# Kernel tuning notes

Measured on AMD Instinct MI355X. Metric: run time of the kernel, lower is better.

The kernel has to match this reference:

```python
import jax, jax.numpy as jnp
import numpy as np

B, C, H, W = 16, 256, 128, 512
MINW, MINH, AF, HS = 128, 32, 256, 256


def _conv1d(x, w, b, pad):
    # x (B, Cin, L), w (Cout, Cin, K) -> (B, Cout, L)
    y = jax.lax.conv_general_dilated(x, w, (1,), [(pad, pad)],
                                     dimension_numbers=('NCH', 'OIH', 'NCH'))
    return y + b[None, :, None]


def setup_inputs() -> dict:
    key = jax.random.key(0)
    ks = jax.random.split(key, 22)
    def p(i, shape, s=0.05):
        return jax.random.normal(ks[i], shape, jnp.float32) * s
    return dict(
        features=jax.random.normal(ks[0], (B, C, H, W), jnp.float32),
        prev_attn_weights=jax.random.uniform(ks[1], (B, H), jnp.float32),
        coverage_vector=jax.random.uniform(ks[2], (B, H), jnp.float32) * 2.0,
        hidden=jax.random.normal(ks[3], (2, 1, B, HS), jnp.float32),
        dw_w=p(4, (MINW, 1)), dw_b=p(5, (1,)),
        enc_w=p(6, (C, AF)), enc_b=p(7, (AF,)),
        conv_w=p(8, (16, 2, 15)), conv_b=p(9, (16,)),
        dcb_w=p(10, (16, AF)), dcb_b=p(11, (AF,)),
        hid_w=p(12, (HS, AF)), hid_b=p(13, (AF,)),
        align_w=p(14, (AF, 1)), align_b=p(15, (1,)),
        convd_w=p(16, (AF, AF, 5)), convd_b=p(17, (AF,)),
        dh_w=p(18, (MINH, 1)), dh_b=p(19, (1,)),
        dec_w=p(20, (HS + AF, 2)), dec_b=p(21, (2,)),
    )


def reference(features, prev_attn_weights, coverage_vector, hidden,
              dw_w, dw_b, enc_w, enc_b, conv_w, conv_b, dcb_w, dcb_b,
              hid_w, hid_b, align_w, align_b, convd_w, convd_b,
              dh_w, dh_b, dec_w, dec_b):
    b, c, h, w = features.shape
    # AdaptiveMaxPool2d((None, MINW)): W divisible by MINW -> uniform windows
    pooled = features.reshape(b, c, h, MINW, w // MINW).max(-1)   # (B,C,H,MINW)
    h_feat = (pooled @ dw_w + dw_b)[..., 0]                       # (B,C,H)
    s = jnp.einsum('bch,cf->bhf', h_feat, enc_w) + enc_b          # (B,H,AF)
    # location + clamped coverage, InstanceNorm1d (no affine, eps=1e-5)
    cat = jnp.stack([prev_attn_weights,
                     jnp.clip(coverage_vector, 0.0, 1.0)], axis=1)  # (B,2,H)
    mu = cat.mean(-1, keepdims=True)
    var = cat.var(-1, keepdims=True)
    cat = (cat - mu) * jax.lax.rsqrt(var + 1e-5)
    cb = _conv1d(cat, conv_w, conv_b, 7)                          # (B,16,H)
    s = s + jnp.einsum('bkh,kf->bhf', cb, dcb_w) + dcb_b
    hh = hidden[0]                                                # (1,B,HS) = LSTM h
    s = s + (jnp.einsum('lbh,hf->lbf', hh, hid_w) + hid_b).transpose(1, 0, 2)  # (B,1,AF) bcast
    s = jnp.tanh(s)
    align = s @ align_w + align_b                                 # (B,H,1)
    attn = jax.nn.softmax(align, axis=1)[..., 0]                  # (B,H)
    context = jnp.einsum('bchw,bh->bcw', features, attn)          # (B,C,W)
    # learned stop decision
    d = jax.nn.relu(_conv1d(s.transpose(0, 2, 1), convd_w, convd_b, 2))  # (B,AF,H)
    d = d.reshape(b, AF, MINH, h // MINH).max(-1)                 # AdaptiveMaxPool1d(MINH)
    d = jax.nn.relu(d @ dh_w + dh_b)[..., 0]                      # (B,AF)
    d = jnp.concatenate([hh[0], d], axis=1)                       # (B,HS+AF)
    decision = d @ dec_w + dec_b                                  # (B,2)
    return context, attn, decision
```

## Files before the change

### kernel.cpp

```cpp
#include <hip/hip_runtime.h>
#include <hip/hip_bf16.h>
#include <math.h>

#define B_ 16
#define C_ 256
#define H_ 128
#define W_ 512
#define AF_ 256
#define HS_ 256

__global__ void k_pre(const float* __restrict__ convd_w,
                      const float* __restrict__ hidden,
                      const float* __restrict__ hid_w,
                      const float* __restrict__ hid_b,
                      float* __restrict__ w2, float* __restrict__ hv) {
  int bid = blockIdx.x, tid = threadIdx.x;
  if (bid < 256) {
    int f = bid;
#pragma unroll
    for (int q = 0; q < 5; ++q) {
      int r = q * 256 + tid;
      w2[(size_t)r * 256 + f] = convd_w[(size_t)f * 1280 + r];
    }
  } else {
    int b = bid - 256;
    const float* hh = hidden + b * HS_;
    float acc = hid_b[tid];
    for (int k = 0; k < HS_; ++k) acc = fmaf(hh[k], hid_w[k * AF_ + tid], acc);
    hv[b * AF_ + tid] = acc;
  }
}

__global__ void k_pool(const float* __restrict__ feat,
                       const float* __restrict__ dw_w,
                       const float* __restrict__ dw_b,
                       float* __restrict__ hf) {
  int gid = blockIdx.x * blockDim.x + threadIdx.x;
  int wid = gid >> 6;
  int lane = threadIdx.x & 63;
  const float4* row = reinterpret_cast<const float4*>(feat) + (size_t)wid * 128;
  float4 a = row[lane];
  float4 b = row[lane + 64];
  float m0 = fmaxf(fmaxf(a.x, a.y), fmaxf(a.z, a.w));
  float m1 = fmaxf(fmaxf(b.x, b.y), fmaxf(b.z, b.w));
  float p = m0 * dw_w[lane] + m1 * dw_w[lane + 64];
#pragma unroll
  for (int off = 32; off > 0; off >>= 1) p += __shfl_down(p, off, 64);
  if (lane == 0) hf[wid] = p + dw_b[0];
}

__global__ void k_sbuild(const float* __restrict__ pa,
                         const float* __restrict__ cv,
                         const float* __restrict__ hf,
                         const float* __restrict__ enc_w, const float* __restrict__ enc_b,
                         const float* __restrict__ conv_w, const float* __restrict__ conv_b,
                         const float* __restrict__ dcb_w, const float* __restrict__ dcb_b,
                         const float* __restrict__ hv,
                         const float* __restrict__ align_w, const float* __restrict__ align_b,
                         float* __restrict__ sbuf, float* __restrict__ alignv) {
  __shared__ float cat[2][H_];
  __shared__ float stats[4];
  __shared__ float cbl[4][16];
  __shared__ float red[4][4];
  int bidx = blockIdx.x;
  int b = bidx >> 5;
  int h0 = (bidx & 31) * 4;
  int tid = threadIdx.x;

  if (tid < H_) {
    cat[0][tid] = pa[b * H_ + tid];
    float x = cv[b * H_ + tid];
    cat[1][tid] = fminf(fmaxf(x, 0.f), 1.f);
  }
  __syncthreads();
  if (tid < 2) {
    float s = 0.f, s2 = 0.f;
    for (int t = 0; t < H_; ++t) { float x = cat[tid][t]; s += x; s2 += x * x; }
    float mu = s / (float)H_;
    float var = s2 / (float)H_ - mu * mu;
    stats[tid * 2] = mu;
    stats[tid * 2 + 1] = rsqrtf(var + 1e-5f);
  }
  __syncthreads();
  {
    int ch = tid >> 7, t = tid & 127;
    cat[ch][t] = (cat[ch][t] - stats[ch * 2]) * stats[ch * 2 + 1];
  }
  __syncthreads();
  if (tid < 64) {
    int k = tid & 15, j = tid >> 4;
    int h = h0 + j;
    float acc = conv_b[k];
    for (int c2 = 0; c2 < 2; ++c2)
      for (int t = 0; t < 15; ++t) {
        int hh = h + t - 7;
        if (hh >= 0 && hh < H_) acc += cat[c2][hh] * conv_w[(k * 2 + c2) * 15 + t];
      }
    cbl[j][k] = acc;
  }
  __syncthreads();

  int f = tid;
  float base = enc_b[f] + dcb_b[f] + hv[b * AF_ + f];
  float acc[4];
#pragma unroll
  for (int j = 0; j < 4; ++j) {
    float a = base;
#pragma unroll
    for (int k = 0; k < 16; ++k) a = fmaf(cbl[j][k], dcb_w[k * AF_ + f], a);
    acc[j] = a;
  }
  const float* hfb = hf + (size_t)(b * C_) * H_ + h0;
  for (int c = 0; c < C_; ++c) {
    float w = enc_w[c * AF_ + f];
#pragma unroll
    for (int j = 0; j < 4; ++j) acc[j] = fmaf(hfb[c * H_ + j], w, acc[j]);
  }
  float aw = align_w[f];
  int wvi = tid >> 6, lane = tid & 63;
#pragma unroll
  for (int j = 0; j < 4; ++j) {
    float s = tanhf(acc[j]);
    sbuf[(size_t)(b * H_ + h0 + j) * AF_ + f] = s;
    float v = s * aw;
#pragma unroll
    for (int off = 32; off > 0; off >>= 1) v += __shfl_down(v, off, 64);
    if (lane == 0) red[wvi][j] = v;
  }
  __syncthreads();
  if (tid < 4)
    alignv[b * H_ + h0 + tid] =
        red[0][tid] + red[1][tid] + red[2][tid] + red[3][tid] + align_b[0];
}

__global__ void k_softmax(const float* __restrict__ alignv, float* __restrict__ attn) {
  __shared__ float redm[2], reds[2];
  int b = blockIdx.x, t = threadIdx.x;
  float v = alignv[b * H_ + t];
  float m = v;
#pragma unroll
  for (int off = 32; off > 0; off >>= 1) m = fmaxf(m, __shfl_down(m, off, 64));
  if ((t & 63) == 0) redm[t >> 6] = m;
  __syncthreads();
  float mm = fmaxf(redm[0], redm[1]);
  float e = expf(v - mm);
  float s = e;
#pragma unroll
  for (int off = 32; off > 0; off >>= 1) s += __shfl_down(s, off, 64);
  if ((t & 63) == 0) reds[t >> 6] = s;
  __syncthreads();
  attn[b * H_ + t] = e / (reds[0] + reds[1]);
}

__global__ void k_dconv(const float* __restrict__ sbuf, const float* __restrict__ w2,
                        const float* __restrict__ convd_b, float* __restrict__ dpool) {
  __shared__ float sw[12][AF_];
  __shared__ float part[8][AF_];
  int bidx = blockIdx.x;
  int b = bidx >> 4;
  int h0 = (bidx & 15) * 8;
  int tid = threadIdx.x;
  int f = tid & 255;
  int chalf = tid >> 8;
  for (int rr = chalf; rr < 12; rr += 2) {
    int h = h0 - 2 + rr;
    sw[rr][f] = (h >= 0 && h < H_) ? sbuf[(size_t)(b * H_ + h) * AF_ + f] : 0.f;
  }
  __syncthreads();
  float acc[8];
#pragma unroll
  for (int j = 0; j < 8; ++j) acc[j] = 0.f;
  int cstart = chalf * 128;
  for (int c = cstart; c < cstart + 128; ++c) {
    float sr[12];
#pragma unroll
    for (int rr = 0; rr < 12; ++rr) sr[rr] = sw[rr][c];
    const float* wp = w2 + (size_t)c * 5 * 256 + f;
#pragma unroll
    for (int t = 0; t < 5; ++t) {
      float wv = wp[t * 256];
#pragma unroll
      for (int j = 0; j < 8; ++j) acc[j] = fmaf(sr[j + t], wv, acc[j]);
    }
  }
  if (chalf == 1) {
#pragma unroll
    for (int j = 0; j < 8; ++j) part[j][f] = acc[j];
  }
  __syncthreads();
  if (chalf == 0) {
    float bias = convd_b[f];
#pragma unroll
    for (int j = 0; j < 8; ++j) acc[j] = fmaxf(acc[j] + part[j][f] + bias, 0.f);
    float p0 = fmaxf(fmaxf(acc[0], acc[1]), fmaxf(acc[2], acc[3]));
    float p1 = fmaxf(fmaxf(acc[4], acc[5]), fmaxf(acc[6], acc[7]));
    int m0 = h0 >> 2;
    dpool[(size_t)(b * 32 + m0) * AF_ + f] = p0;
    dpool[(size_t)(b * 32 + m0 + 1) * AF_ + f] = p1;
  }
}

__global__ void k_decision(const float* __restrict__ dpool, const float* __restrict__ hidden,
                           const float* __restrict__ dh_w, const float* __restrict__ dh_b,
                           const float* __restrict__ dec_w, const float* __restrict__ dec_b,
                           float* __restrict__ dec_out) {
  __shared__ float ddl[AF_];
  __shared__ float red[4];
  int b = blockIdx.x, tid = threadIdx.x;
  float acc = dh_b[0];
  for (int m = 0; m < 32; ++m) acc = fmaf(dpool[(size_t)(b * 32 + m) * AF_ + tid], dh_w[m], acc);
  ddl[tid] = fmaxf(acc, 0.f);
  __syncthreads();
  int col = tid >> 7, kk = tid & 127;
  float a = 0.f;
#pragma unroll
  for (int q = 0; q < 4; ++q) {
    int idx = kk + 128 * q;
    float x = (idx < 256) ? hidden[b * HS_ + idx] : ddl[idx - 256];
    a = fmaf(x, dec_w[idx * 2 + col], a);
  }
#pragma unroll
  for (int off = 32; off > 0; off >>= 1) a += __shfl_down(a, off, 64);
  if ((tid & 63) == 0) red[tid >> 6] = a;
  __syncthreads();
  if (tid < 2) dec_out[b * 2 + tid] = red[tid * 2] + red[tid * 2 + 1] + dec_b[tid];
}

__global__ void k_context(const float* __restrict__ feat, const float* __restrict__ attn,
                          float* __restrict__ ctx) {
  __shared__ float at[H_];
  int cb = 2047 - blockIdx.x;
  int b = cb >> 7;
  int c0 = (cb & 127) * 2;
  int tid = threadIdx.x;
  if (tid < H_) at[tid] = attn[b * H_ + tid];
  __syncthreads();
  int c = c0 + (tid >> 7);
  int wq = tid & 127;
  const float4* f4 = reinterpret_cast<const float4*>(feat) +
                     (size_t)(b * C_ + c) * H_ * (W_ / 4) + wq;
  float4 acc = make_float4(0.f, 0.f, 0.f, 0.f);
  for (int h = 0; h < H_; ++h) {
    float4 x = f4[(size_t)h * (W_ / 4)];
    float a = at[h];
    acc.x += x.x * a; acc.y += x.y * a; acc.z += x.z * a; acc.w += x.w * a;
  }
  reinterpret_cast<float4*>(ctx)[(size_t)(b * C_ + c) * (W_ / 4) + wq] = acc;
}

extern "C" void kernel_launch(void* const* d_in, const int* in_sizes, int n_in,
                              void* d_out, int out_size, void* d_ws, size_t ws_size,
                              hipStream_t stream) {
  const float* feat    = (const float*)d_in[0];
  const float* pa      = (const float*)d_in[1];
  const float* cv      = (const float*)d_in[2];
  const float* hidden  = (const float*)d_in[3];
  const float* dw_w    = (const float*)d_in[4];
  const float* dw_b    = (const float*)d_in[5];
  const float* enc_w   = (const float*)d_in[6];
  const float* enc_b   = (const float*)d_in[7];
  const float* conv_w  = (const float*)d_in[8];
  const float* conv_b  = (const float*)d_in[9];
  const float* dcb_w   = (const float*)d_in[10];
  const float* dcb_b   = (const float*)d_in[11];
  const float* hid_w   = (const float*)d_in[12];
  const float* hid_b   = (const float*)d_in[13];
  const float* align_w = (const float*)d_in[14];
  const float* align_b = (const float*)d_in[15];
  const float* convd_w = (const float*)d_in[16];
  const float* convd_b = (const float*)d_in[17];
  const float* dh_w    = (const float*)d_in[18];
  const float* dh_b    = (const float*)d_in[19];
  const float* dec_w   = (const float*)d_in[20];
  const float* dec_b   = (const float*)d_in[21];

  float* out  = (float*)d_out;
  float* ctx  = out;
  float* attn = out + 2097152;
  float* dec  = out + 2097152 + 2048;

  float* hf     = ctx;
  float* sbuf   = ctx + 524288;
  float* dpool  = ctx + 1048576;
  float* hv     = ctx + 1179648;
  float* alignv = ctx + 1183744;
  float* w2     = ctx + 1185792;

  k_pre<<<272, 256, 0, stream>>>(convd_w, hidden, hid_w, hid_b, w2, hv);
  k_pool<<<131072, 256, 0, stream>>>(feat, dw_w, dw_b, hf);
  k_sbuild<<<512, 256, 0, stream>>>(pa, cv, hf, enc_w, enc_b, conv_w, conv_b,
                                    dcb_w, dcb_b, hv, align_w, align_b, sbuf, alignv);
  k_softmax<<<16, 128, 0, stream>>>(alignv, attn);
  k_dconv<<<256, 512, 0, stream>>>(sbuf, w2, convd_b, dpool);
  k_decision<<<16, 256, 0, stream>>>(dpool, hidden, dh_w, dh_b, dec_w, dec_b, dec);
  k_context<<<2048, 256, 0, stream>>>(feat, attn, ctx);
}
```

Before: 439.6 us.

## Fuse independent kernels into combined launches and use nontemporal feature loads

```diff
diff --git a/kernel.cpp b/kernel.cpp
--- a/kernel.cpp
+++ b/kernel.cpp
@@ -9,11 +9,17 @@
 #define AF_ 256
 #define HS_ 256
 
-__global__ void k_pre(const float* __restrict__ convd_w,
-                      const float* __restrict__ hidden,
-                      const float* __restrict__ hid_w,
-                      const float* __restrict__ hid_b,
-                      float* __restrict__ w2, float* __restrict__ hv) {
+typedef float f4v __attribute__((ext_vector_type(4)));
+
+__global__ void k_pre_pool(const float* __restrict__ feat,
+                           const float* __restrict__ dw_w,
+                           const float* __restrict__ dw_b,
+                           const float* __restrict__ convd_w,
+                           const float* __restrict__ hidden,
+                           const float* __restrict__ hid_w,
+                           const float* __restrict__ hid_b,
+                           float* __restrict__ hf, float* __restrict__ w2,
+                           float* __restrict__ hv) {
   int bid = blockIdx.x, tid = threadIdx.x;
   if (bid < 256) {
     int f = bid;
@@ -22,31 +28,25 @@
       int r = q * 256 + tid;
       w2[(size_t)r * 256 + f] = convd_w[(size_t)f * 1280 + r];
     }
-  } else {
+  } else if (bid < 272) {
     int b = bid - 256;
     const float* hh = hidden + b * HS_;
     float acc = hid_b[tid];
     for (int k = 0; k < HS_; ++k) acc = fmaf(hh[k], hid_w[k * AF_ + tid], acc);
     hv[b * AF_ + tid] = acc;
-  }
-}
-
-__global__ void k_pool(const float* __restrict__ feat,
-                       const float* __restrict__ dw_w,
-                       const float* __restrict__ dw_b,
-                       float* __restrict__ hf) {
-  int gid = blockIdx.x * blockDim.x + threadIdx.x;
-  int wid = gid >> 6;
-  int lane = threadIdx.x & 63;
-  const float4* row = reinterpret_cast<const float4*>(feat) + (size_t)wid * 128;
-  float4 a = row[lane];
-  float4 b = row[lane + 64];
-  float m0 = fmaxf(fmaxf(a.x, a.y), fmaxf(a.z, a.w));
-  float m1 = fmaxf(fmaxf(b.x, b.y), fmaxf(b.z, b.w));
-  float p = m0 * dw_w[lane] + m1 * dw_w[lane + 64];
-#pragma unroll
-  for (int off = 32; off > 0; off >>= 1) p += __shfl_down(p, off, 64);
-  if (lane == 0) hf[wid] = p + dw_b[0];
+  } else {
+    int wid = (bid - 272) * 4 + (tid >> 6);
+    int lane = tid & 63;
+    const f4v* row = reinterpret_cast<const f4v*>(feat) + (size_t)wid * 128;
+    f4v a = __builtin_nontemporal_load(row + lane);
+    f4v b = __builtin_nontemporal_load(row + lane + 64);
+    float m0 = fmaxf(fmaxf(a.x, a.y), fmaxf(a.z, a.w));
+    float m1 = fmaxf(fmaxf(b.x, b.y), fmaxf(b.z, b.w));
+    float p = m0 * dw_w[lane] + m1 * dw_w[lane + 64];
+#pragma unroll
+    for (int off = 32; off > 0; off >>= 1) p += __shfl_down(p, off, 64);
+    if (lane == 0) hf[wid] = p + dw_b[0];
+  }
 }
 
 __global__ void k_sbuild(const float* __restrict__ pa,
@@ -133,119 +133,129 @@
         red[0][tid] + red[1][tid] + red[2][tid] + red[3][tid] + align_b[0];
 }
 
-__global__ void k_softmax(const float* __restrict__ alignv, float* __restrict__ attn) {
-  __shared__ float redm[2], reds[2];
-  int b = blockIdx.x, t = threadIdx.x;
-  float v = alignv[b * H_ + t];
-  float m = v;
-#pragma unroll
-  for (int off = 32; off > 0; off >>= 1) m = fmaxf(m, __shfl_down(m, off, 64));
-  if ((t & 63) == 0) redm[t >> 6] = m;
-  __syncthreads();
-  float mm = fmaxf(redm[0], redm[1]);
-  float e = expf(v - mm);
-  float s = e;
-#pragma unroll
-  for (int off = 32; off > 0; off >>= 1) s += __shfl_down(s, off, 64);
-  if ((t & 63) == 0) reds[t >> 6] = s;
-  __syncthreads();
-  attn[b * H_ + t] = e / (reds[0] + reds[1]);
-}
-
-__global__ void k_dconv(const float* __restrict__ sbuf, const float* __restrict__ w2,
-                        const float* __restrict__ convd_b, float* __restrict__ dpool) {
+__global__ void k_sm_dconv(const float* __restrict__ sbuf, const float* __restrict__ w2,
+                           const float* __restrict__ convd_b,
+                           const float* __restrict__ alignv,
+                           float* __restrict__ dpool, float* __restrict__ attn) {
   __shared__ float sw[12][AF_];
   __shared__ float part[8][AF_];
+  __shared__ float redm[8], reds[8];
   int bidx = blockIdx.x;
-  int b = bidx >> 4;
-  int h0 = (bidx & 15) * 8;
   int tid = threadIdx.x;
-  int f = tid & 255;
-  int chalf = tid >> 8;
-  for (int rr = chalf; rr < 12; rr += 2) {
-    int h = h0 - 2 + rr;
-    sw[rr][f] = (h >= 0 && h < H_) ? sbuf[(size_t)(b * H_ + h) * AF_ + f] : 0.f;
-  }
-  __syncthreads();
-  float acc[8];
-#pragma unroll
-  for (int j = 0; j < 8; ++j) acc[j] = 0.f;
-  int cstart = chalf * 128;
-  for (int c = cstart; c < cstart + 128; ++c) {
-    float sr[12];
-#pragma unroll
-    for (int rr = 0; rr < 12; ++rr) sr[rr] = sw[rr][c];
-    const float* wp = w2 + (size_t)c * 5 * 256 + f;
-#pragma unroll
-    for (int t = 0; t < 5; ++t) {
-      float wv = wp[t * 256];
-#pragma unroll
-      for (int j = 0; j < 8; ++j) acc[j] = fmaf(sr[j + t], wv, acc[j]);
-    }
-  }
-  if (chalf == 1) {
-#pragma unroll
-    for (int j = 0; j < 8; ++j) part[j][f] = acc[j];
-  }
-  __syncthreads();
-  if (chalf == 0) {
-    float bias = convd_b[f];
-#pragma unroll
-    for (int j = 0; j < 8; ++j) acc[j] = fmaxf(acc[j] + part[j][f] + bias, 0.f);
-    float p0 = fmaxf(fmaxf(acc[0], acc[1]), fmaxf(acc[2], acc[3]));
-    float p1 = fmaxf(fmaxf(acc[4], acc[5]), fmaxf(acc[6], acc[7]));
-    int m0 = h0 >> 2;
-    dpool[(size_t)(b * 32 + m0) * AF_ + f] = p0;
-    dpool[(size_t)(b * 32 + m0 + 1) * AF_ + f] = p1;
-  }
-}
-
-__global__ void k_decision(const float* __restrict__ dpool, const float* __restrict__ hidden,
-                           const float* __restrict__ dh_w, const float* __restrict__ dh_b,
-                           const float* __restrict__ dec_w, const float* __restrict__ dec_b,
-                           float* __restrict__ dec_out) {
+  if (bidx < 256) {
+    int b = bidx >> 4;
+    int h0 = (bidx & 15) * 8;
+    int f = tid & 255;
+    int chalf = tid >> 8;
+    for (int rr = chalf; rr < 12; rr += 2) {
+      int h = h0 - 2 + rr;
+      sw[rr][f] = (h >= 0 && h < H_) ? sbuf[(size_t)(b * H_ + h) * AF_ + f] : 0.f;
+    }
+    __syncthreads();
+    float acc[8];
+#pragma unroll
+    for (int j = 0; j < 8; ++j) acc[j] = 0.f;
+    int cstart = chalf * 128;
+    for (int c = cstart; c < cstart + 128; ++c) {
+      float sr[12];
+#pragma unroll
+      for (int rr = 0; rr < 12; ++rr) sr[rr] = sw[rr][c];
+      const float* wp = w2 + (size_t)c * 5 * 256 + f;
+#pragma unroll
+      for (int t = 0; t < 5; ++t) {
+        float wv = wp[t * 256];
+#pragma unroll
+        for (int j = 0; j < 8; ++j) acc[j] = fmaf(sr[j + t], wv, acc[j]);
+      }
+    }
+    if (chalf == 1) {
+#pragma unroll
+      for (int j = 0; j < 8; ++j) part[j][f] = acc[j];
+    }
+    __syncthreads();
+    if (chalf == 0) {
+      float bias = convd_b[f];
+#pragma unroll
+      for (int j = 0; j < 8; ++j) acc[j] = fmaxf(acc[j] + part[j][f] + bias, 0.f);
+      float p0 = fmaxf(fmaxf(acc[0], acc[1]), fmaxf(acc[2], acc[3]));
+      float p1 = fmaxf(fmaxf(acc[4], acc[5]), fmaxf(acc[6], acc[7]));
+      int m0 = h0 >> 2;
+      dpool[(size_t)(b * 32 + m0) * AF_ + f] = p0;
+      dpool[(size_t)(b * 32 + m0 + 1) * AF_ + f] = p1;
+    }
+  } else {
+    int b = bidx - 256;
+    float v = (tid < H_) ? alignv[b * H_ + tid] : -1e30f;
+    float m = v;
+#pragma unroll
+    for (int off = 32; off > 0; off >>= 1) m = fmaxf(m, __shfl_down(m, off, 64));
+    if ((tid & 63) == 0) redm[tid >> 6] = m;
+    __syncthreads();
+    float mm = redm[0];
+#pragma unroll
+    for (int q = 1; q < 8; ++q) mm = fmaxf(mm, redm[q]);
+    float e = expf(v - mm);
+    float s = e;
+#pragma unroll
+    for (int off = 32; off > 0; off >>= 1) s += __shfl_down(s, off, 64);
+    if ((tid & 63) == 0) reds[tid >> 6] = s;
+    __syncthreads();
+    float S = 0.f;
+#pragma unroll
+    for (int q = 0; q < 8; ++q) S += reds[q];
+    if (tid < H_) attn[b * H_ + tid] = e / S;
+  }
+}
+
+__global__ void k_dec_ctx(const float* __restrict__ feat, const float* __restrict__ attn,
+                          const float* __restrict__ dpool, const float* __restrict__ hidden,
+                          const float* __restrict__ dh_w, const float* __restrict__ dh_b,
+                          const float* __restrict__ dec_w, const float* __restrict__ dec_b,
+                          float* __restrict__ dec_out, float* __restrict__ ctx) {
+  __shared__ float at[H_];
   __shared__ float ddl[AF_];
   __shared__ float red[4];
-  int b = blockIdx.x, tid = threadIdx.x;
-  float acc = dh_b[0];
-  for (int m = 0; m < 32; ++m) acc = fmaf(dpool[(size_t)(b * 32 + m) * AF_ + tid], dh_w[m], acc);
-  ddl[tid] = fmaxf(acc, 0.f);
-  __syncthreads();
-  int col = tid >> 7, kk = tid & 127;
-  float a = 0.f;
-#pragma unroll
-  for (int q = 0; q < 4; ++q) {
-    int idx = kk + 128 * q;
-    float x = (idx < 256) ? hidden[b * HS_ + idx] : ddl[idx - 256];
-    a = fmaf(x, dec_w[idx * 2 + col], a);
-  }
-#pragma unroll
-  for (int off = 32; off > 0; off >>= 1) a += __shfl_down(a, off, 64);
-  if ((tid & 63) == 0) red[tid >> 6] = a;
-  __syncthreads();
-  if (tid < 2) dec_out[b * 2 + tid] = red[tid * 2] + red[tid * 2 + 1] + dec_b[tid];
-}
-
-__global__ void k_context(const float* __restrict__ feat, const float* __restrict__ attn,
-                          float* __restrict__ ctx) {
-  __shared__ float at[H_];
-  int cb = 2047 - blockIdx.x;
-  int b = cb >> 7;
-  int c0 = (cb & 127) * 2;
+  int bidx = blockIdx.x;
   int tid = threadIdx.x;
-  if (tid < H_) at[tid] = attn[b * H_ + tid];
-  __syncthreads();
-  int c = c0 + (tid >> 7);
-  int wq = tid & 127;
-  const float4* f4 = reinterpret_cast<const float4*>(feat) +
-                     (size_t)(b * C_ + c) * H_ * (W_ / 4) + wq;
-  float4 acc = make_float4(0.f, 0.f, 0.f, 0.f);
-  for (int h = 0; h < H_; ++h) {
-    float4 x = f4[(size_t)h * (W_ / 4)];
-    float a = at[h];
-    acc.x += x.x * a; acc.y += x.y * a; acc.z += x.z * a; acc.w += x.w * a;
-  }
-  reinterpret_cast<float4*>(ctx)[(size_t)(b * C_ + c) * (W_ / 4) + wq] = acc;
+  if (bidx < 16) {
+    int b = bidx;
+    float acc = dh_b[0];
+    for (int m = 0; m < 32; ++m)
+      acc = fmaf(dpool[(size_t)(b * 32 + m) * AF_ + tid], dh_w[m], acc);
+    ddl[tid] = fmaxf(acc, 0.f);
+    __syncthreads();
+    int col = tid >> 7, kk = tid & 127;
+    float a = 0.f;
+#pragma unroll
+    for (int q = 0; q < 4; ++q) {
+      int idx = kk + 128 * q;
+      float x = (idx < 256) ? hidden[b * HS_ + idx] : ddl[idx - 256];
+      a = fmaf(x, dec_w[idx * 2 + col], a);
+    }
+#pragma unroll
+    for (int off = 32; off > 0; off >>= 1) a += __shfl_down(a, off, 64);
+    if ((tid & 63) == 0) red[tid >> 6] = a;
+    __syncthreads();
+    if (tid < 2) dec_out[b * 2 + tid] = red[tid * 2] + red[tid * 2 + 1] + dec_b[tid];
+  } else {
+    int cb = 2063 - bidx;
+    int b = cb >> 7;
+    int c0 = (cb & 127) * 2;
+    if (tid < H_) at[tid] = attn[b * H_ + tid];
+    __syncthreads();
+    int c = c0 + (tid >> 7);
+    int wq = tid & 127;
+    const f4v* f4 = reinterpret_cast<const f4v*>(feat) +
+                    (size_t)(b * C_ + c) * H_ * (W_ / 4) + wq;
+    f4v acc = (f4v){0.f, 0.f, 0.f, 0.f};
+    for (int h = 0; h < H_; ++h) {
+      f4v x = __builtin_nontemporal_load(f4 + (size_t)h * (W_ / 4));
+      float a = at[h];
+      acc.x += x.x * a; acc.y += x.y * a; acc.z += x.z * a; acc.w += x.w * a;
+    }
+    __builtin_nontemporal_store(acc,
+        reinterpret_cast<f4v*>(ctx) + (size_t)(b * C_ + c) * (W_ / 4) + wq);
+  }
 }
 
 extern "C" void kernel_launch(void* const* d_in, const int* in_sizes, int n_in,
@@ -281,17 +291,16 @@
 
   float* hf     = ctx;
   float* sbuf   = ctx + 524288;
-  float* dpool  = ctx + 1048576;
   float* hv     = ctx + 1179648;
   float* alignv = ctx + 1183744;
   float* w2     = ctx + 1185792;
-
-  k_pre<<<272, 256, 0, stream>>>(convd_w, hidden, hid_w, hid_b, w2, hv);
-  k_pool<<<131072, 256, 0, stream>>>(feat, dw_w, dw_b, hf);
+  float* dpool  = (float*)d_ws;
+
+  k_pre_pool<<<131344, 256, 0, stream>>>(feat, dw_w, dw_b, convd_w, hidden,
+                                         hid_w, hid_b, hf, w2, hv);
   k_sbuild<<<512, 256, 0, stream>>>(pa, cv, hf, enc_w, enc_b, conv_w, conv_b,
                                     dcb_w, dcb_b, hv, align_w, align_b, sbuf, alignv);
-  k_softmax<<<16, 128, 0, stream>>>(alignv, attn);
-  k_dconv<<<256, 512, 0, stream>>>(sbuf, w2, convd_b, dpool);
-  k_decision<<<16, 256, 0, stream>>>(dpool, hidden, dh_w, dh_b, dec_w, dec_b, dec);
-  k_context<<<2048, 256, 0, stream>>>(feat, attn, ctx);
-}
+  k_sm_dconv<<<272, 512, 0, stream>>>(sbuf, w2, convd_b, alignv, dpool, attn);
+  k_dec_ctx<<<2064, 256, 0, stream>>>(feat, attn, dpool, hidden, dh_w, dh_b,
+                                      dec_w, dec_b, dec, ctx);
+}
```

After: 394.7 us. 1.11x faster.
